# Performance work log

Measured on AMD Instinct MI355X. Metric: run time of the kernel, lower is better.

## Reference

```python
import jax, jax.numpy as jnp
import numpy as np

PAD = 1  # padding from init_kwargs

def setup_inputs() -> dict:
    key = jax.random.key(0)
    k1, k2 = jax.random.split(key)
    x = jax.random.normal(k1, (1, 256, 224, 224), dtype=jnp.float32)
    # Conv2d_mvm weight: [out_channels, in_channels, kh, kw]
    weight = jax.random.normal(k2, (256, 256, 3, 3), dtype=jnp.float32) * 0.05
    return {"x": x, "weight": weight}

def reference(x, weight):
    # Exact math of the bit-sliced crossbar conv forward: stride-1 cross-correlation
    # with zero padding, no bias, output squeezed to [C_out, H_out, W_out]
    # (the original forward emits no batch dimension).
    out = jax.lax.conv_general_dilated(
        x, weight,
        window_strides=(1, 1),
        padding=((PAD, PAD), (PAD, PAD)),
        dimension_numbers=("NCHW", "OIHW", "NCHW"),
    )
    return out[0]  # [C_out, H_out, W_out]
```

## Files before the change

kernel.cpp:

```cpp
#include <hip/hip_runtime.h>


#define H 224
#define W 224
#define NPOS (H*W)
#define CI 256
#define CO 256
#define KDIM 2304
#define HP 226
#define XP_ELEMS (HP*HP*CI)
#define AP_ELEMS (CO*KDIM)

typedef __bf16 bf16x8 __attribute__((ext_vector_type(8)));
typedef float f32x4 __attribute__((ext_vector_type(4)));
typedef unsigned short u16x4 __attribute__((ext_vector_type(4)));
typedef unsigned short u16x8 __attribute__((ext_vector_type(8)));

__device__ __forceinline__ unsigned short f2bf(float f) {
    unsigned int u = __float_as_uint(f);
    u += 0x7fff + ((u >> 16) & 1);
    return (unsigned short)(u >> 16);
}

__device__ __forceinline__ void load_lds16(const unsigned short* g, unsigned short* l) {
    __builtin_amdgcn_global_load_lds(
        (const __attribute__((address_space(1))) void*)g,
        (__attribute__((address_space(3))) void*)l,
        16, 0, 0);
}

#define XT_BLOCKS 3136
#define WT_BLOCKS 256
#define BORDER_V8 28800
#define ROW_V8 7232
__global__ void prep_kernel(const float* __restrict__ x, const float* __restrict__ w,
                            unsigned short* __restrict__ ap, unsigned short* __restrict__ xp) {
    __shared__ unsigned short smem[64 * 68];
    const int bx = blockIdx.x;
    const int t = threadIdx.x;

    if (bx < XT_BLOCKS) {
        const unsigned int pBase = (unsigned int)(bx % 784) * 64;
        const unsigned int ciBase = (unsigned int)(bx / 784) * 64;
        {
            const int p4 = (t & 15) * 4;
            const int c0 = t >> 4;
#pragma unroll
            for (int i = 0; i < 4; ++i) {
                const int ci_l = c0 + i * 16;
                const f32x4 v = *(const f32x4*)&x[(ciBase + ci_l) * NPOS + pBase + p4];
                u16x4 s;
                s[0] = f2bf(v[0]); s[1] = f2bf(v[1]); s[2] = f2bf(v[2]); s[3] = f2bf(v[3]);
                *(u16x4*)&smem[ci_l * 68 + p4] = s;
            }
        }
        __syncthreads();
        {
            const int ci0 = (t & 7) * 8;
            const int pr = t >> 3;
#pragma unroll
            for (int j = 0; j < 2; ++j) {
                const int p_l = pr + j * 32;
                const unsigned int p = pBase + p_l;
                const unsigned int hi = p / W, wi = p - hi * W;
                u16x8 v;
#pragma unroll
                for (int k = 0; k < 8; ++k) v[k] = smem[(ci0 + k) * 68 + p_l];
                *(u16x8*)&xp[((hi + 1) * HP + (wi + 1)) * CI + ciBase + ci0] = v;
            }
        }
    } else if (bx < XT_BLOCKS + WT_BLOCKS) {
        const int co = bx - XT_BLOCKS;
        const float* wc = w + co * KDIM;
#pragma unroll
        for (int i = 0; i < 9; ++i)
            smem[i * 256 + t] = f2bf(wc[i * 256 + t]);
        __syncthreads();
        unsigned short* apc = ap + co * KDIM;
#pragma unroll
        for (int tap = 0; tap < 9; ++tap)
            apc[tap * 256 + t] = smem[t * 9 + tap];
    } else {
        const int idx = (bx - XT_BLOCKS - WT_BLOCKS) * 256 + t;
        if (idx < BORDER_V8) {
            unsigned short* p;
            if (idx < 2 * ROW_V8) {
                const int r = idx / ROW_V8;
                const int off = idx - r * ROW_V8;
                p = xp + r * (225 * HP * CI) + off * 8;
            } else {
                const int i2 = idx - 2 * ROW_V8;
                const int seg = i2 >> 5;
                const int o = i2 & 31;
                const int hp = 1 + (seg >> 1);
                const int wp = (seg & 1) * 225;
                p = xp + (hp * HP + wp) * CI + o * 8;
            }
            *(u16x8*)p = (u16x8){0, 0, 0, 0, 0, 0, 0, 0};
        }
    }
}


#define RDALL(base)                                                             \
    _Pragma("unroll")                                                           \
    for (int mi = 0; mi < 4; ++mi)                                              \
        afA[mi] = *(const bf16x8*)&lds[(base) + arow + mi * 512];               \
    _Pragma("unroll")                                                           \
    for (int mi = 0; mi < 4; ++mi)                                              \
        afB[mi] = *(const bf16x8*)&lds[(base) + arow + (4 + mi) * 512];         \
    _Pragma("unroll")                                                           \
    for (int ni = 0; ni < 4; ++ni)                                              \
        bfr[ni] = *(const bf16x8*)&lds[(base) + brow + ni * 512];

#define MMH(half, afX)                                                          \
    __builtin_amdgcn_s_setprio(1);                                              \
    _Pragma("unroll")                                                           \
    for (int mi = 0; mi < 4; ++mi)                                              \
        _Pragma("unroll")                                                       \
        for (int ni = 0; ni < 4; ++ni)                                          \
            acc[(half) * 4 + mi][ni] = __builtin_amdgcn_mfma_f32_16x16x32_bf16( \
                afX[mi], bfr[ni], acc[(half) * 4 + mi][ni], 0, 0, 0);           \
    __builtin_amdgcn_s_setprio(0);

__global__ __launch_bounds__(512, 1) void gemm_conv_kernel(
    const unsigned short* __restrict__ Ap,
    const unsigned short* __restrict__ Xp,
    float* __restrict__ out)
{
    __shared__ unsigned short lds[65536];

    const int tid = threadIdx.x;
    const int Nb = blockIdx.x;
    const int wave = tid >> 6;
    const int wm = wave >> 2;
    const int wn = wave & 3;
    const int lane = tid & 63;
    const int ln15 = lane & 15;
    const int quad = lane >> 4;
    const int slot8 = (quad ^ ((ln15 >> 1) & 3)) * 8;
    const int arow = (wm * 128 + ln15) * 32 + slot8;
    const int brow = 32768 + (wn * 64 + ln15) * 32 + slot8;

    const int c4 = (tid & 3) ^ ((tid >> 3) & 3);
    const unsigned short* a_src[2];
    const unsigned short* b_src[2];
#pragma unroll
    for (int j = 0; j < 2; ++j) {
        const int r = j * 128 + (tid >> 2);
        a_src[j] = Ap + r * KDIM + c4 * 8;
        unsigned int p = Nb * 256 + r;
        unsigned int hi = p / W, wi = p - hi * W;
        b_src[j] = Xp + (hi * HP + wi) * CI + c4 * 8;
    }

    f32x4 acc[8][4];
#pragma unroll
    for (int mi = 0; mi < 8; ++mi)
#pragma unroll
        for (int ni = 0; ni < 4; ++ni)
            acc[mi][ni] = (f32x4){0.f, 0.f, 0.f, 0.f};

    auto stageA = [&](int kt, int k) {
        const int dst = ((kt & 1) * 2 + k) * 8192;
        const int off = kt * 64 + k * 32;
#pragma unroll
        for (int j = 0; j < 2; ++j)
            load_lds16(a_src[j] + off, &lds[dst + (j * 8 + wave) * 512]);
    };
    auto stageB = [&](int kt, int k) {
        const int dst = 32768 + ((kt & 1) * 2 + k) * 8192;
        const int tap = kt >> 2;
        const int dh = (tap * 11) >> 5;
        const int dw = tap - dh * 3;
        const int off = (dh * HP + dw) * CI + (kt & 3) * 64 + k * 32;
#pragma unroll
        for (int j = 0; j < 2; ++j)
            load_lds16(b_src[j] + off, &lds[dst + (j * 8 + wave) * 512]);
    };
    auto stage8 = [&](int kt) {
        stageA(kt, 0); stageB(kt, 0);
        stageA(kt, 1); stageB(kt, 1);
    };

    bf16x8 afA[4], afB[4], bfr[4];

    stage8(0);
    asm volatile("s_waitcnt vmcnt(4)" ::: "memory");
    __builtin_amdgcn_s_barrier();

    for (int kt = 0; kt < 36; ++kt) {
        const int b0 = (kt & 1) * 16384;
        const int b1 = b0 + 8192;
        const bool st = kt < 35;
        if (st) stage8(kt + 1);
        RDALL(b0)
        MMH(0, afA)
        MMH(1, afB)
        if (st) asm volatile("s_waitcnt vmcnt(8)" ::: "memory");
        else    asm volatile("s_waitcnt vmcnt(0)" ::: "memory");
        __builtin_amdgcn_s_barrier();
        RDALL(b1)
        MMH(0, afA)
        MMH(1, afB)
        if (st) {
            asm volatile("s_waitcnt vmcnt(4)" ::: "memory");
            __builtin_amdgcn_s_barrier();
        }
    }

    const int pcol = Nb * 256 + wn * 64 + ln15;
    const int corow = wm * 128 + quad * 4;
#pragma unroll
    for (int mi = 0; mi < 8; ++mi)
#pragma unroll
        for (int ni = 0; ni < 4; ++ni)
#pragma unroll
            for (int r = 0; r < 4; ++r)
                out[(corow + mi * 16 + r) * NPOS + pcol + ni * 16] = acc[mi][ni][r];
}

extern "C" void kernel_launch(void* const* d_in, const int* in_sizes, int n_in,
                              void* d_out, int out_size, void* d_ws, size_t ws_size,
                              hipStream_t stream) {
    const float* x = (const float*)d_in[0];
    const float* w = (const float*)d_in[1];
    float* out = (float*)d_out;

    unsigned short* xp = (unsigned short*)d_ws;
    unsigned short* ap = xp + XP_ELEMS;

    prep_kernel<<<XT_BLOCKS + WT_BLOCKS + 113, 256, 0, stream>>>(x, w, ap, xp);
    gemm_conv_kernel<<<dim3(NPOS / 256), 512, 0, stream>>>(ap, xp, out);
}
```

Before: 165.5 us.

## Use a four-slot LDS ring with double-buffered register fragments in conv GEMM

Restructures the GEMM main loop so each K-step of 32 lands in one of four LDS slots, with global-to-LDS loads issued three steps ahead. Register fragments are double-buffered, so the LDS reads for the next step are issued while the MFMAs for the current step run. The goal is to hide LDS read latency and global load latency behind matrix math, and to replace the previous pattern of a wait plus barrier in the middle of each 64-wide step. The cost is more VGPRs for the second fragment set and more intricate control of vmcnt waits and barriers near the end of the loop.

```diff
diff --git a/kernel.cpp b/kernel.cpp
--- a/kernel.cpp
+++ b/kernel.cpp
@@ -102,25 +102,22 @@
 }
 
 
-#define RDALL(base)                                                             \
+#define READF(afX, bfX, base)                                                   \
     _Pragma("unroll")                                                           \
-    for (int mi = 0; mi < 4; ++mi)                                              \
-        afA[mi] = *(const bf16x8*)&lds[(base) + arow + mi * 512];               \
-    _Pragma("unroll")                                                           \
-    for (int mi = 0; mi < 4; ++mi)                                              \
-        afB[mi] = *(const bf16x8*)&lds[(base) + arow + (4 + mi) * 512];         \
+    for (int mi = 0; mi < 8; ++mi)                                              \
+        afX[mi] = *(const bf16x8*)&lds[(base) + arow + mi * 512];               \
     _Pragma("unroll")                                                           \
     for (int ni = 0; ni < 4; ++ni)                                              \
-        bfr[ni] = *(const bf16x8*)&lds[(base) + brow + ni * 512];
-
-#define MMH(half, afX)                                                          \
+        bfX[ni] = *(const bf16x8*)&lds[(base) + brow + ni * 512];
+
+#define MFMA32(afX, bfX)                                                        \
     __builtin_amdgcn_s_setprio(1);                                              \
     _Pragma("unroll")                                                           \
-    for (int mi = 0; mi < 4; ++mi)                                              \
+    for (int mi = 0; mi < 8; ++mi)                                              \
         _Pragma("unroll")                                                       \
         for (int ni = 0; ni < 4; ++ni)                                          \
-            acc[(half) * 4 + mi][ni] = __builtin_amdgcn_mfma_f32_16x16x32_bf16( \
-                afX[mi], bfr[ni], acc[(half) * 4 + mi][ni], 0, 0, 0);           \
+            acc[mi][ni] = __builtin_amdgcn_mfma_f32_16x16x32_bf16(              \
+                afX[mi], bfX[ni], acc[mi][ni], 0, 0, 0);                        \
     __builtin_amdgcn_s_setprio(0);
 
 __global__ __launch_bounds__(512, 1) void gemm_conv_kernel(
@@ -128,7 +125,7 @@
     const unsigned short* __restrict__ Xp,
     float* __restrict__ out)
 {
-    __shared__ unsigned short lds[65536];
+    __shared__ unsigned short lds[32768 * 2];
 
     const int tid = threadIdx.x;
     const int Nb = blockIdx.x;
@@ -161,50 +158,44 @@
         for (int ni = 0; ni < 4; ++ni)
             acc[mi][ni] = (f32x4){0.f, 0.f, 0.f, 0.f};
 
-    auto stageA = [&](int kt, int k) {
-        const int dst = ((kt & 1) * 2 + k) * 8192;
-        const int off = kt * 64 + k * 32;
-#pragma unroll
-        for (int j = 0; j < 2; ++j)
-            load_lds16(a_src[j] + off, &lds[dst + (j * 8 + wave) * 512]);
-    };
-    auto stageB = [&](int kt, int k) {
-        const int dst = 32768 + ((kt & 1) * 2 + k) * 8192;
-        const int tap = kt >> 2;
+    auto stageT = [&](int kt) {
+        const int da = (kt & 3) * 8192;
+        const int db = 32768 + (kt & 3) * 8192;
+        const int aoff = kt * 32;
+        const int tap = kt >> 3;
         const int dh = (tap * 11) >> 5;
         const int dw = tap - dh * 3;
-        const int off = (dh * HP + dw) * CI + (kt & 3) * 64 + k * 32;
-#pragma unroll
-        for (int j = 0; j < 2; ++j)
-            load_lds16(b_src[j] + off, &lds[dst + (j * 8 + wave) * 512]);
+        const int boff = (dh * HP + dw) * CI + (kt & 7) * 32;
+#pragma unroll
+        for (int j = 0; j < 2; ++j) {
+            load_lds16(a_src[j] + aoff, &lds[da + (j * 8 + wave) * 512]);
+            load_lds16(b_src[j] + boff, &lds[db + (j * 8 + wave) * 512]);
+        }
     };
-    auto stage8 = [&](int kt) {
-        stageA(kt, 0); stageB(kt, 0);
-        stageA(kt, 1); stageB(kt, 1);
-    };
-
-    bf16x8 afA[4], afB[4], bfr[4];
-
-    stage8(0);
+
+    bf16x8 af0[8], bf0[4], af1[8], bf1[4];
+
+    stageT(0); stageT(1); stageT(2);
     asm volatile("s_waitcnt vmcnt(4)" ::: "memory");
     __builtin_amdgcn_s_barrier();
-
-    for (int kt = 0; kt < 36; ++kt) {
-        const int b0 = (kt & 1) * 16384;
-        const int b1 = b0 + 8192;
-        const bool st = kt < 35;
-        if (st) stage8(kt + 1);
-        RDALL(b0)
-        MMH(0, afA)
-        MMH(1, afB)
-        if (st) asm volatile("s_waitcnt vmcnt(8)" ::: "memory");
-        else    asm volatile("s_waitcnt vmcnt(0)" ::: "memory");
-        __builtin_amdgcn_s_barrier();
-        RDALL(b1)
-        MMH(0, afA)
-        MMH(1, afB)
-        if (st) {
+    READF(af0, bf0, 0)
+
+    for (int kt = 0; kt < 72; kt += 2) {
+        if (kt <= 68) stageT(kt + 3);
+        READF(af1, bf1, ((kt + 1) & 3) * 8192)
+        MFMA32(af0, bf0)
+        if (kt <= 68) {
             asm volatile("s_waitcnt vmcnt(4)" ::: "memory");
+            __builtin_amdgcn_s_barrier();
+        }
+        if (kt + 1 <= 68) stageT(kt + 4);
+        if (kt + 1 < 71) { READF(af0, bf0, ((kt + 2) & 3) * 8192) }
+        MFMA32(af1, bf1)
+        if (kt + 1 <= 68) {
+            asm volatile("s_waitcnt vmcnt(4)" ::: "memory");
+            __builtin_amdgcn_s_barrier();
+        } else if (kt + 1 == 69) {
+            asm volatile("s_waitcnt vmcnt(0)" ::: "memory");
             __builtin_amdgcn_s_barrier();
         }
     }
```

Measured after the change: 160.3 us. -3.1%, faster.
